# Kernel optimization log

Measured on AMD Instinct MI355X. Metric: run time of the kernel, lower is better.

## Reference

```python
import jax, jax.numpy as jnp
import numpy as np

DIM = 1024
N_HEADS = 16
HEAD_DIM = DIM // N_HEADS
SCALE = HEAD_DIM ** (-0.5)


def setup_inputs() -> dict:
    key = jax.random.key(0)
    ks = jax.random.split(key, 5)
    B, N = 2, 1024
    x = jax.random.normal(ks[0], (B, N, DIM), dtype=jnp.float32)
    # torch nn.Linear convention: weight is (out_features, in_features)
    w_qkvg = jax.random.normal(ks[1], (4 * DIM, DIM), dtype=jnp.float32) * (DIM ** -0.5)
    b_qkvg = jax.random.normal(ks[2], (4 * DIM,), dtype=jnp.float32) * 0.02
    w_proj = jax.random.normal(ks[3], (DIM, DIM), dtype=jnp.float32) * (DIM ** -0.5)
    b_proj = jax.random.normal(ks[4], (DIM,), dtype=jnp.float32) * 0.02
    return {"x": x, "w_qkvg": w_qkvg, "b_qkvg": b_qkvg, "w_proj": w_proj, "b_proj": b_proj}


def reference(x, w_qkvg, b_qkvg, w_proj, b_proj):
    B, N, dim = x.shape
    # fused qkvg projection: (B, N, 4*dim)
    qkvg = x @ w_qkvg.T + b_qkvg
    # (B, N, 4, H, hd) -> (4, B, H, N, hd)
    qkvg = qkvg.reshape(B, N, 4, N_HEADS, HEAD_DIM).transpose(2, 0, 3, 1, 4)
    q = jax.nn.softplus(qkvg[0])          # (B, H, N, hd)
    k = jax.nn.softplus(qkvg[1])          # (B, H, N, hd)
    v = jax.nn.gelu(qkvg[2], approximate=False)  # (B, H, N, hd)
    g = jax.nn.gelu(qkvg[3], approximate=False)  # (B, H, N, hd)
    # kv = k @ v^T over head_dim -> (B, H, N, N)
    kv = jnp.einsum('bhnd,bhmd->bhnm', k, v)
    # z: contract q over tokens with per-token k-sums -> (B, H, hd)
    z = jnp.einsum('bhcn,bhc->bhn', q, k.sum(axis=-1)) * SCALE
    z = 1.0 / (z + dim)
    # out[b,h,d,n] = sum_c q[b,h,c,n] * kv[b,h,c,d] -> (B, H, N, hd)
    out = jnp.einsum('bhcn,bhcd->bhdn', q, kv) * SCALE
    out = (out + v) * z[:, :, None, :]    # broadcast z over token axis
    out = out.reshape(B, N, dim)          # raw reshape, faithful to original
    out = out * g.reshape(B, N, dim)
    out = out @ w_proj.T + b_proj
    return out
```

## Files before the change

### kernel.cpp

```cpp
#include <hip/hip_runtime.h>
#include <hip/hip_bf16.h>
#include <math.h>

typedef float f32x4 __attribute__((ext_vector_type(4)));
typedef __bf16 bf16_t;
typedef bf16_t bf16x8 __attribute__((ext_vector_type(8)));
typedef bf16_t bf16x4 __attribute__((ext_vector_type(4)));

__device__ __forceinline__ void gload_lds16(const bf16_t* g, bf16_t* l) {
    __builtin_amdgcn_global_load_lds(
        (const __attribute__((address_space(1))) unsigned int*)g,
        (__attribute__((address_space(3))) unsigned int*)l, 16, 0, 0);
}

template<int N_IMM>
__device__ __forceinline__ void wait_vmcnt() {
    if constexpr (N_IMM == 0) asm volatile("s_waitcnt vmcnt(0)" ::: "memory");
    else if constexpr (N_IMM == 1) asm volatile("s_waitcnt vmcnt(1)" ::: "memory");
    else if constexpr (N_IMM == 2) asm volatile("s_waitcnt vmcnt(2)" ::: "memory");
    else if constexpr (N_IMM == 3) asm volatile("s_waitcnt vmcnt(3)" ::: "memory");
    else if constexpr (N_IMM == 4) asm volatile("s_waitcnt vmcnt(4)" ::: "memory");
    else static_assert(N_IMM <= 4, "unsupported vmcnt");
}

__global__ __launch_bounds__(256) void cvt3(const float* __restrict__ a, bf16_t* __restrict__ ao, int na4,
                                            const float* __restrict__ b, bf16_t* __restrict__ bo, int nb4,
                                            const float* __restrict__ c, bf16_t* __restrict__ co, int nc4) {
    int q = blockIdx.x * 256 + threadIdx.x;
    const float* src; bf16_t* dst;
    if (q < na4)            { src = a + (size_t)q * 4;              dst = ao + (size_t)q * 4; }
    else if (q < na4 + nb4) { int r = q - na4; src = b + (size_t)r * 4; dst = bo + (size_t)r * 4; }
    else if (q < na4 + nb4 + nc4) { int r = q - na4 - nb4; src = c + (size_t)r * 4; dst = co + (size_t)r * 4; }
    else return;
    float4 v = *reinterpret_cast<const float4*>(src);
    bf16x4 o;
    o[0] = (bf16_t)v.x; o[1] = (bf16_t)v.y; o[2] = (bf16_t)v.z; o[3] = (bf16_t)v.w;
    *reinterpret_cast<bf16x4*>(dst) = o;
}

template<int BM, int BN, int MR, int NR, int EPI>
__global__ __launch_bounds__(256) void gemm_bt(const bf16_t* __restrict__ A,
                                               const bf16_t* __restrict__ B,
                                               const float* __restrict__ bias,
                                               void* __restrict__ Cout,
                                               int M, int N, int K) {
    constexpr int WCOLS = BN / (NR * 16);
    constexpr int WROWS = BM / (MR * 16);
    static_assert(WROWS * WCOLS == 4, "4 waves");
    constexpr int ASEG = BM / 64, BSEG = BN / 64;
    constexpr int LOADS = ASEG + BSEG;
    __shared__ bf16_t As[2][BM * 32];
    __shared__ bf16_t Bs[2][BN * 32];
    const int tid = threadIdx.x;
    const int lane = tid & 63;
    const int w = tid >> 6;
    const int wr = w / WCOLS, wc = w % WCOLS;
    const int NTM = M / BM;
    const int bid = blockIdx.x;
    const int m0 = (bid % NTM) * BM, n0 = (bid / NTM) * BN;
    const int l15 = lane & 15, lg = lane >> 4;
    const int srow = lane >> 2, pos = lane & 3;

    f32x4 acc[MR][NR] = {};
    const int TNUM = K / 32;

    auto stage = [&](int buf, int k0) {
#pragma unroll
        for (int t = 0; t < ASEG; ++t) {
            int s = w + t * 4;
            int row = s * 16 + srow;
            int ch = pos ^ ((row >> 1) & 3);
            gload_lds16(&A[(size_t)(m0 + row) * K + k0 + ch * 8], &As[buf][s * 512]);
        }
#pragma unroll
        for (int t = 0; t < BSEG; ++t) {
            int s = w + t * 4;
            int row = s * 16 + srow;
            int ch = pos ^ ((row >> 1) & 3);
            gload_lds16(&B[(size_t)(n0 + row) * K + k0 + ch * 8], &Bs[buf][s * 512]);
        }
    };

    stage(0, 0);
    int cur = 0;
    for (int t = 0; t < TNUM; ++t) {
        if (t + 1 < TNUM) {
            stage(cur ^ 1, (t + 1) * 32);
            wait_vmcnt<LOADS>();
        } else {
            wait_vmcnt<0>();
        }
        __builtin_amdgcn_s_barrier();
        __builtin_amdgcn_sched_barrier(0);

        const bf16_t* Ac = As[cur];
        const bf16_t* Bc = Bs[cur];
        bf16x8 af[MR], bfr[NR];
#pragma unroll
        for (int i = 0; i < MR; ++i) {
            int ar = wr * MR * 16 + i * 16 + l15;
            af[i] = *(const bf16x8*)(&Ac[ar * 32 + (lg ^ ((ar >> 1) & 3)) * 8]);
        }
#pragma unroll
        for (int j = 0; j < NR; ++j) {
            int br = wc * NR * 16 + j * 16 + l15;
            bfr[j] = *(const bf16x8*)(&Bc[br * 32 + (lg ^ ((br >> 1) & 3)) * 8]);
        }
#pragma unroll
        for (int i = 0; i < MR; ++i)
#pragma unroll
            for (int j = 0; j < NR; ++j)
                acc[i][j] = __builtin_amdgcn_mfma_f32_16x16x32_bf16(af[i], bfr[j], acc[i][j], 0, 0, 0);
        __builtin_amdgcn_sched_barrier(0);
        __builtin_amdgcn_s_barrier();
        cur ^= 1;
    }

#pragma unroll
    for (int i = 0; i < MR; ++i) {
        int gm_base = m0 + wr * MR * 16 + i * 16 + lg * 4;
#pragma unroll
        for (int j = 0; j < NR; ++j) {
            int gn = n0 + wc * NR * 16 + j * 16 + l15;
            float bv = bias[gn];
#pragma unroll
            for (int r = 0; r < 4; ++r) {
                int gm = gm_base + r;
                float v = acc[i][j][r] + bv;
                if (EPI == 0) {
                    float a;
                    if ((gn >> 10) < 2) {
                        a = fmaxf(v, 0.f) + log1pf(expf(-fabsf(v)));
                    } else {
                        a = 0.5f * v * (1.f + erff(v * 0.70710678118654752f));
                    }
                    ((bf16_t*)Cout)[(size_t)gm * N + gn] = (bf16_t)a;
                } else {
                    ((float*)Cout)[(size_t)gm * N + gn] = v;
                }
            }
        }
    }
}

__global__ __launch_bounds__(256) void attn_A(const bf16_t* __restrict__ qkvg,
                                              float* __restrict__ Apart) {
    const int bh = blockIdx.x;
    const int p = blockIdx.y;
    const int b = bh >> 4, h = bh & 15;
    const int tid = threadIdx.x;
    __shared__ float ks[32][64];
    __shared__ float qs[32][64];
    float acc[4][4] = {};
    const int dg = tid >> 4, eg = tid & 15;
    const int stok = tid >> 3, se0 = (tid & 7) * 8;
    const size_t base = ((size_t)b * 1024) * 4096 + (size_t)h * 64;

    for (int t0 = p * 128; t0 < p * 128 + 128; t0 += 32) {
        __syncthreads();
        size_t rowb = base + (size_t)(t0 + stok) * 4096;
        bf16x8 qv8 = *(const bf16x8*)(&qkvg[rowb + se0]);
        bf16x8 kv8 = *(const bf16x8*)(&qkvg[rowb + 1024 + se0]);
#pragma unroll
        for (int jj = 0; jj < 8; ++jj) {
            qs[stok][se0 + jj] = (float)qv8[jj];
            ks[stok][se0 + jj] = (float)kv8[jj];
        }
        __syncthreads();
#pragma unroll 8
        for (int tt = 0; tt < 32; ++tt) {
            f32x4 kv = *(const f32x4*)(&ks[tt][dg * 4]);
            f32x4 qv = *(const f32x4*)(&qs[tt][eg * 4]);
#pragma unroll
            for (int i = 0; i < 4; ++i)
#pragma unroll
                for (int j = 0; j < 4; ++j) acc[i][j] += kv[i] * qv[j];
        }
    }
    float* dst = Apart + ((size_t)p * 32 + bh) * 4096;
#pragma unroll
    for (int i = 0; i < 4; ++i)
#pragma unroll
        for (int j = 0; j < 4; ++j)
            dst[(dg * 4 + i) * 64 + eg * 4 + j] = acc[i][j];
}

__global__ __launch_bounds__(256) void reduce_A_z(const float* __restrict__ Apart,
                                                  float* __restrict__ A,
                                                  float* __restrict__ z) {
    const int bh = blockIdx.x;
    const int tid = threadIdx.x;
    __shared__ float As[4096];
    for (int i0 = tid * 4; i0 < 4096; i0 += 1024) {
        f32x4 s = {};
#pragma unroll
        for (int p = 0; p < 8; ++p) {
            f32x4 v = *(const f32x4*)(&Apart[((size_t)p * 32 + bh) * 4096 + i0]);
            s += v;
        }
        *(f32x4*)(&As[i0]) = s;
        *(f32x4*)(&A[(size_t)bh * 4096 + i0]) = s;
    }
    __syncthreads();
    if (tid < 64) {
        float s = 0.f;
#pragma unroll 8
        for (int d = 0; d < 64; ++d) s += As[d * 64 + tid];
        z[bh * 64 + tid] = 1.0f / (s * 0.125f + 1024.0f);
    }
}

__global__ __launch_bounds__(256) void out_Y(const bf16_t* __restrict__ qkvg,
                                             const float* __restrict__ A,
                                             const float* __restrict__ z,
                                             bf16_t* __restrict__ Y) {
    const int bh = blockIdx.x;
    const int b = bh >> 4, h = bh & 15;
    const int chunk = blockIdx.y;
    const int tid = threadIdx.x;
    __shared__ float As[64][64];
    __shared__ float vs[32][64];
    __shared__ float zs[64];
    for (int i = tid; i < 4096; i += 256) As[i >> 6][i & 63] = A[(size_t)bh * 4096 + i];
    if (tid < 64) zs[tid] = z[bh * 64 + tid];
    const size_t base = ((size_t)b * 1024) * 4096 + (size_t)h * 64;
    const int e = tid & 63, trow = tid >> 6;
    const int stok = tid >> 3, se0 = (tid & 7) * 8;

    for (int t0 = chunk * 64; t0 < chunk * 64 + 64; t0 += 32) {
        __syncthreads();
        bf16x8 vv8 = *(const bf16x8*)(&qkvg[base + (size_t)(t0 + stok) * 4096 + 2048 + se0]);
#pragma unroll
        for (int jj = 0; jj < 8; ++jj) vs[stok][se0 + jj] = (float)vv8[jj];
        __syncthreads();
#pragma unroll
        for (int kk = 0; kk < 8; ++kk) {
            int ml = trow * 8 + kk;
            int m = t0 + ml;
            float s = 0.f;
#pragma unroll 8
            for (int d = 0; d < 64; ++d) s += vs[ml][d] * As[d][e];
            float g = (float)qkvg[base + (size_t)m * 4096 + 3072 + e];
            float o = (s * 0.125f + vs[ml][e]) * zs[e] * g;
            Y[((size_t)b * 1024 + h * 64 + (m >> 4)) * 1024 + ((m & 15) << 6) + e] = (bf16_t)o;
        }
    }
}

extern "C" void kernel_launch(void* const* d_in, const int* in_sizes, int n_in,
                              void* d_out, int out_size, void* d_ws, size_t ws_size,
                              hipStream_t stream) {
    const float* x      = (const float*)d_in[0];
    const float* w_qkvg = (const float*)d_in[1];
    const float* b_qkvg = (const float*)d_in[2];
    const float* w_proj = (const float*)d_in[3];
    const float* b_proj = (const float*)d_in[4];

    char* p = (char*)d_ws;
    bf16_t* xb    = (bf16_t*)p; p += (size_t)2048 * 1024 * 2;
    bf16_t* w1b   = (bf16_t*)p; p += (size_t)4096 * 1024 * 2;
    bf16_t* w2b   = (bf16_t*)p; p += (size_t)1024 * 1024 * 2;
    bf16_t* qkvg  = (bf16_t*)p; p += (size_t)2048 * 4096 * 2;
    float*  Apart = (float*)p;  p += (size_t)8 * 32 * 4096 * 4;
    float*  Afull = (float*)p;  p += (size_t)32 * 4096 * 4;
    float*  zbuf  = (float*)p;  p += (size_t)32 * 64 * 4;
    bf16_t* Ybuf  = (bf16_t*)p; p += (size_t)2048 * 1024 * 2;

    cvt3<<<7168, 256, 0, stream>>>(x, xb, 524288, w_qkvg, w1b, 1048576, w_proj, w2b, 262144);

    gemm_bt<128, 64, 4, 2, 0><<<16 * 64, 256, 0, stream>>>(xb, w1b, b_qkvg, (void*)qkvg, 2048, 4096, 1024);
    attn_A<<<dim3(32, 8), 256, 0, stream>>>(qkvg, Apart);
    reduce_A_z<<<32, 256, 0, stream>>>(Apart, Afull, zbuf);
    out_Y<<<dim3(32, 16), 256, 0, stream>>>(qkvg, Afull, zbuf, Ybuf);
    gemm_bt<64, 64, 2, 2, 1><<<32 * 16, 256, 0, stream>>>(Ybuf, w2b, b_proj, d_out, 2048, 1024, 1024);
}
```

Before: 101.8 us.

## Deepen GEMM pipeline to four LDS stages, swizzle block order, enlarge QKVG tile

The GEMM's double-buffered LDS pipeline becomes a four-buffer ring that prefetches three K-steps ahead. It waits on vmcnt for the oldest stage and drops the trailing barrier per iteration. Block indices are remapped into 8x8 tile groups so neighbouring blocks share A/B rows in L2. The QKVG projection tile grows from 128x64 to 128x128, which raises register and LDS use per block and may lower occupancy.

New measurement: 158.4 us. 55.6% more time.

```diff
diff --git a/kernel.cpp b/kernel.cpp
--- a/kernel.cpp
+++ b/kernel.cpp
@@ -20,7 +20,10 @@
     else if constexpr (N_IMM == 2) asm volatile("s_waitcnt vmcnt(2)" ::: "memory");
     else if constexpr (N_IMM == 3) asm volatile("s_waitcnt vmcnt(3)" ::: "memory");
     else if constexpr (N_IMM == 4) asm volatile("s_waitcnt vmcnt(4)" ::: "memory");
-    else static_assert(N_IMM <= 4, "unsupported vmcnt");
+    else if constexpr (N_IMM == 6) asm volatile("s_waitcnt vmcnt(6)" ::: "memory");
+    else if constexpr (N_IMM == 8) asm volatile("s_waitcnt vmcnt(8)" ::: "memory");
+    else if constexpr (N_IMM == 12) asm volatile("s_waitcnt vmcnt(12)" ::: "memory");
+    else static_assert(N_IMM == 0, "unsupported vmcnt");
 }
 
 __global__ __launch_bounds__(256) void cvt3(const float* __restrict__ a, bf16_t* __restrict__ ao, int na4,
@@ -49,15 +52,21 @@
     static_assert(WROWS * WCOLS == 4, "4 waves");
     constexpr int ASEG = BM / 64, BSEG = BN / 64;
     constexpr int LOADS = ASEG + BSEG;
-    __shared__ bf16_t As[2][BM * 32];
-    __shared__ bf16_t Bs[2][BN * 32];
+    __shared__ bf16_t As[4][BM * 32];
+    __shared__ bf16_t Bs[4][BN * 32];
     const int tid = threadIdx.x;
     const int lane = tid & 63;
     const int w = tid >> 6;
     const int wr = w / WCOLS, wc = w % WCOLS;
+
     const int NTM = M / BM;
-    const int bid = blockIdx.x;
-    const int m0 = (bid % NTM) * BM, n0 = (bid / NTM) * BN;
+    const int c = blockIdx.x & 7;
+    const int pp = blockIdx.x >> 3;
+    const int CHM = NTM >> 3;
+    const int cm = c % CHM, cn = c / CHM;
+    const int mt = cm * 8 + (pp & 7), nt = cn * 8 + (pp >> 3);
+    const int m0 = mt * BM, n0 = nt * BN;
+
     const int l15 = lane & 15, lg = lane >> 4;
     const int srow = lane >> 2, pos = lane & 3;
 
@@ -81,20 +90,18 @@
         }
     };
 
-    stage(0, 0);
-    int cur = 0;
+    stage(0, 0); stage(1, 32); stage(2, 64);
     for (int t = 0; t < TNUM; ++t) {
-        if (t + 1 < TNUM) {
-            stage(cur ^ 1, (t + 1) * 32);
-            wait_vmcnt<LOADS>();
-        } else {
-            wait_vmcnt<0>();
-        }
+        int rem = TNUM - 1 - t;
+        if (rem >= 2)       wait_vmcnt<2 * LOADS>();
+        else if (rem == 1)  wait_vmcnt<LOADS>();
+        else                wait_vmcnt<0>();
         __builtin_amdgcn_s_barrier();
         __builtin_amdgcn_sched_barrier(0);
-
-        const bf16_t* Ac = As[cur];
-        const bf16_t* Bc = Bs[cur];
+        if (t + 3 < TNUM) stage((t + 3) & 3, (t + 3) * 32);
+
+        const bf16_t* Ac = As[t & 3];
+        const bf16_t* Bc = Bs[t & 3];
         bf16x8 af[MR], bfr[NR];
 #pragma unroll
         for (int i = 0; i < MR; ++i) {
@@ -112,8 +119,6 @@
             for (int j = 0; j < NR; ++j)
                 acc[i][j] = __builtin_amdgcn_mfma_f32_16x16x32_bf16(af[i], bfr[j], acc[i][j], 0, 0, 0);
         __builtin_amdgcn_sched_barrier(0);
-        __builtin_amdgcn_s_barrier();
-        cur ^= 1;
     }
 
 #pragma unroll
@@ -268,9 +273,9 @@
 
     cvt3<<<7168, 256, 0, stream>>>(x, xb, 524288, w_qkvg, w1b, 1048576, w_proj, w2b, 262144);
 
-    gemm_bt<128, 64, 4, 2, 0><<<16 * 64, 256, 0, stream>>>(xb, w1b, b_qkvg, (void*)qkvg, 2048, 4096, 1024);
+    gemm_bt<128, 128, 4, 4, 0><<<512, 256, 0, stream>>>(xb, w1b, b_qkvg, (void*)qkvg, 2048, 4096, 1024);
     attn_A<<<dim3(32, 8), 256, 0, stream>>>(qkvg, Apart);
     reduce_A_z<<<32, 256, 0, stream>>>(Apart, Afull, zbuf);
     out_Y<<<dim3(32, 16), 256, 0, stream>>>(qkvg, Afull, zbuf, Ybuf);
-    gemm_bt<64, 64, 2, 2, 1><<<32 * 16, 256, 0, stream>>>(Ybuf, w2b, b_proj, d_out, 2048, 1024, 1024);
-}
+    gemm_bt<64, 64, 2, 2, 1><<<512, 256, 0, stream>>>(Ybuf, w2b, b_proj, d_out, 2048, 1024, 1024);
+}
```

## Replace QKVG GEMM with 512-thread 128x256 tile kernel and XCD-aware block mapping

Applied to the files above, without the earlier changes.

Adds a dedicated gemm8 kernel for the QKVG projection. It uses 8 waves, 128x256 output tiles and a K-step of 64 with an XOR-swizzled LDS layout, so each block reuses its operands across more MFMAs and fewer blocks are launched. Both GEMMs now remap block IDs so that the blocks landing on each of the 8 XCDs cover a contiguous sub-grid of tiles, which is meant to improve L2 locality. The risks are higher register and LDS pressure, which lowers occupancy, and only 256 blocks on the large GEMM, which may leave some CUs underused.

Result: slower. 155.2 us (+52.4%).

```diff
diff --git a/kernel.cpp b/kernel.cpp
--- a/kernel.cpp
+++ b/kernel.cpp
@@ -16,11 +16,10 @@
 template<int N_IMM>
 __device__ __forceinline__ void wait_vmcnt() {
     if constexpr (N_IMM == 0) asm volatile("s_waitcnt vmcnt(0)" ::: "memory");
-    else if constexpr (N_IMM == 1) asm volatile("s_waitcnt vmcnt(1)" ::: "memory");
     else if constexpr (N_IMM == 2) asm volatile("s_waitcnt vmcnt(2)" ::: "memory");
     else if constexpr (N_IMM == 3) asm volatile("s_waitcnt vmcnt(3)" ::: "memory");
     else if constexpr (N_IMM == 4) asm volatile("s_waitcnt vmcnt(4)" ::: "memory");
-    else static_assert(N_IMM <= 4, "unsupported vmcnt");
+    else static_assert(N_IMM == 0, "unsupported vmcnt");
 }
 
 __global__ __launch_bounds__(256) void cvt3(const float* __restrict__ a, bf16_t* __restrict__ ao, int na4,
@@ -38,11 +37,115 @@
     *reinterpret_cast<bf16x4*>(dst) = o;
 }
 
-template<int BM, int BN, int MR, int NR, int EPI>
+__global__ __launch_bounds__(512) void gemm8(const bf16_t* __restrict__ A,
+                                             const bf16_t* __restrict__ B,
+                                             const float* __restrict__ bias,
+                                             bf16_t* __restrict__ Cout,
+                                             int M, int N, int K) {
+    __shared__ bf16_t As[2][128 * 64];
+    __shared__ bf16_t Bs[2][256 * 64];
+    const int tid = threadIdx.x;
+    const int lane = tid & 63;
+    const int w = tid >> 6;
+    const int wr = w >> 2, wc = w & 3;
+
+    const int c = blockIdx.x & 7;
+    const int pp = blockIdx.x >> 3;
+    const int mt = (c & 1) * 8 + (pp & 7);
+    const int nt = (c >> 1) * 4 + (pp >> 3);
+    const int m0 = mt * 128, n0 = nt * 256;
+
+    const int l15 = lane & 15, lg = lane >> 4;
+    const int srow = lane >> 3;
+    const int slot = lane & 7;
+
+    f32x4 acc[4][4] = {};
+    const int TNUM = K / 64;
+
+    auto stage = [&](int buf, int k0) {
+#pragma unroll
+        for (int t = 0; t < 2; ++t) {
+            int s = w + t * 8;
+            int row = s * 8 + srow;
+            int cg = slot ^ (row & 7);
+            gload_lds16(&A[(size_t)(m0 + row) * K + k0 + cg * 8], &As[buf][s * 512]);
+        }
+#pragma unroll
+        for (int t = 0; t < 4; ++t) {
+            int s = w + t * 8;
+            int row = s * 8 + srow;
+            int cg = slot ^ (row & 7);
+            gload_lds16(&B[(size_t)(n0 + row) * K + k0 + cg * 8], &Bs[buf][s * 512]);
+        }
+    };
+
+    stage(0, 0);
+    wait_vmcnt<0>();
+    __builtin_amdgcn_s_barrier();
+    __builtin_amdgcn_sched_barrier(0);
+
+    int cur = 0;
+    for (int t = 0; t < TNUM; ++t) {
+        if (t + 1 < TNUM) stage(cur ^ 1, (t + 1) * 64);
+
+        const bf16_t* Ac = As[cur];
+        const bf16_t* Bc = Bs[cur];
+#pragma unroll
+        for (int kk = 0; kk < 2; ++kk) {
+            bf16x8 af[4], bfr[4];
+#pragma unroll
+            for (int i = 0; i < 4; ++i) {
+                int ar = wr * 64 + i * 16 + l15;
+                int ch = (kk * 4 + lg) ^ (ar & 7);
+                af[i] = *(const bf16x8*)(&Ac[ar * 64 + ch * 8]);
+            }
+#pragma unroll
+            for (int j = 0; j < 4; ++j) {
+                int br = wc * 64 + j * 16 + l15;
+                int ch = (kk * 4 + lg) ^ (br & 7);
+                bfr[j] = *(const bf16x8*)(&Bc[br * 64 + ch * 8]);
+            }
+#pragma unroll
+            for (int i = 0; i < 4; ++i)
+#pragma unroll
+                for (int j = 0; j < 4; ++j)
+                    acc[i][j] = __builtin_amdgcn_mfma_f32_16x16x32_bf16(af[i], bfr[j], acc[i][j], 0, 0, 0);
+        }
+        __builtin_amdgcn_sched_barrier(0);
+        wait_vmcnt<0>();
+        __builtin_amdgcn_s_barrier();
+        __builtin_amdgcn_sched_barrier(0);
+        cur ^= 1;
+    }
+
+#pragma unroll
+    for (int i = 0; i < 4; ++i) {
+        int gm_base = m0 + wr * 64 + i * 16 + lg * 4;
+#pragma unroll
+        for (int j = 0; j < 4; ++j) {
+            int gn = n0 + wc * 64 + j * 16 + l15;
+            float bv = bias[gn];
+#pragma unroll
+            for (int r = 0; r < 4; ++r) {
+                int gm = gm_base + r;
+                float v = acc[i][j][r] + bv;
+                float a;
+                if ((gn >> 10) < 2) {
+                    a = fmaxf(v, 0.f) + log1pf(expf(-fabsf(v)));
+                } else {
+                    a = 0.5f * v * (1.f + erff(v * 0.70710678118654752f));
+                }
+                Cout[(size_t)gm * N + gn] = (bf16_t)a;
+            }
+        }
+    }
+}
+
+template<int BM, int BN, int MR, int NR>
 __global__ __launch_bounds__(256) void gemm_bt(const bf16_t* __restrict__ A,
                                                const bf16_t* __restrict__ B,
                                                const float* __restrict__ bias,
-                                               void* __restrict__ Cout,
+                                               float* __restrict__ Cout,
                                                int M, int N, int K) {
     constexpr int WCOLS = BN / (NR * 16);
     constexpr int WROWS = BM / (MR * 16);
@@ -55,9 +158,16 @@
     const int lane = tid & 63;
     const int w = tid >> 6;
     const int wr = w / WCOLS, wc = w % WCOLS;
-    const int NTM = M / BM;
-    const int bid = blockIdx.x;
-    const int m0 = (bid % NTM) * BM, n0 = (bid / NTM) * BN;
+
+    const int NTM = M / BM, NTN = N / BN;
+    const int CHM = NTM >> 3;
+    const int chunkN = (NTN * CHM) >> 3;
+    const int c = blockIdx.x & 7;
+    const int pp = blockIdx.x >> 3;
+    const int mt = (c % CHM) * 8 + (pp & 7);
+    const int nt = (c / CHM) * chunkN + (pp >> 3);
+    const int m0 = mt * BM, n0 = nt * BN;
+
     const int l15 = lane & 15, lg = lane >> 4;
     const int srow = lane >> 2, pos = lane & 3;
 
@@ -126,18 +236,7 @@
 #pragma unroll
             for (int r = 0; r < 4; ++r) {
                 int gm = gm_base + r;
-                float v = acc[i][j][r] + bv;
-                if (EPI == 0) {
-                    float a;
-                    if ((gn >> 10) < 2) {
-                        a = fmaxf(v, 0.f) + log1pf(expf(-fabsf(v)));
-                    } else {
-                        a = 0.5f * v * (1.f + erff(v * 0.70710678118654752f));
-                    }
-                    ((bf16_t*)Cout)[(size_t)gm * N + gn] = (bf16_t)a;
-                } else {
-                    ((float*)Cout)[(size_t)gm * N + gn] = v;
-                }
+                Cout[(size_t)gm * N + gn] = acc[i][j][r] + bv;
             }
         }
     }
@@ -268,9 +367,9 @@
 
     cvt3<<<7168, 256, 0, stream>>>(x, xb, 524288, w_qkvg, w1b, 1048576, w_proj, w2b, 262144);
 
-    gemm_bt<128, 64, 4, 2, 0><<<16 * 64, 256, 0, stream>>>(xb, w1b, b_qkvg, (void*)qkvg, 2048, 4096, 1024);
+    gemm8<<<256, 512, 0, stream>>>(xb, w1b, b_qkvg, qkvg, 2048, 4096, 1024);
     attn_A<<<dim3(32, 8), 256, 0, stream>>>(qkvg, Apart);
     reduce_A_z<<<32, 256, 0, stream>>>(Apart, Afull, zbuf);
     out_Y<<<dim3(32, 16), 256, 0, stream>>>(qkvg, Afull, zbuf, Ybuf);
-    gemm_bt<64, 64, 2, 2, 1><<<32 * 16, 256, 0, stream>>>(Ybuf, w2b, b_proj, d_out, 2048, 1024, 1024);
-}
+    gemm_bt<64, 64, 2, 2><<<512, 256, 0, stream>>>(Ybuf, w2b, b_proj, (float*)d_out, 2048, 1024, 1024);
+}
```

## Split QKVG GEMM per projection with XCD-aware tile swizzle and specialized epilogues

Applied to the files above, without the earlier changes.

Replaces the single 128x64-tile QKVG GEMM launch with four 64x64-tile launches, one per q/k/v/g slice. Each launch writes into the interleaved output through a new ldc stride and uses a compile-time epilogue (softplus or GELU) in place of a per-element branch. It also remaps block IDs so that each of the 8 blockIdx&7 groups gets a contiguous chunk of M and N tiles, aiming for better L2 locality per XCD. The trade-off is smaller tiles with less operand reuse, plus three extra kernel launches.

After: 131.3 us. 1.29x slower.

```diff
diff --git a/kernel.cpp b/kernel.cpp
--- a/kernel.cpp
+++ b/kernel.cpp
@@ -16,11 +16,10 @@
 template<int N_IMM>
 __device__ __forceinline__ void wait_vmcnt() {
     if constexpr (N_IMM == 0) asm volatile("s_waitcnt vmcnt(0)" ::: "memory");
-    else if constexpr (N_IMM == 1) asm volatile("s_waitcnt vmcnt(1)" ::: "memory");
     else if constexpr (N_IMM == 2) asm volatile("s_waitcnt vmcnt(2)" ::: "memory");
     else if constexpr (N_IMM == 3) asm volatile("s_waitcnt vmcnt(3)" ::: "memory");
     else if constexpr (N_IMM == 4) asm volatile("s_waitcnt vmcnt(4)" ::: "memory");
-    else static_assert(N_IMM <= 4, "unsupported vmcnt");
+    else static_assert(N_IMM == 0, "unsupported vmcnt");
 }
 
 __global__ __launch_bounds__(256) void cvt3(const float* __restrict__ a, bf16_t* __restrict__ ao, int na4,
@@ -43,7 +42,7 @@
                                                const bf16_t* __restrict__ B,
                                                const float* __restrict__ bias,
                                                void* __restrict__ Cout,
-                                               int M, int N, int K) {
+                                               int M, int N, int K, int ldc) {
     constexpr int WCOLS = BN / (NR * 16);
     constexpr int WROWS = BM / (MR * 16);
     static_assert(WROWS * WCOLS == 4, "4 waves");
@@ -55,9 +54,16 @@
     const int lane = tid & 63;
     const int w = tid >> 6;
     const int wr = w / WCOLS, wc = w % WCOLS;
-    const int NTM = M / BM;
-    const int bid = blockIdx.x;
-    const int m0 = (bid % NTM) * BM, n0 = (bid / NTM) * BN;
+
+    const int NTM = M / BM, NTN = N / BN;
+    const int CHM = NTM >> 3;
+    const int chunkN = (NTN * CHM) >> 3;
+    const int c = blockIdx.x & 7;
+    const int pp = blockIdx.x >> 3;
+    const int mt = (c % CHM) * 8 + (pp & 7);
+    const int nt = (c / CHM) * chunkN + (pp >> 3);
+    const int m0 = mt * BM, n0 = nt * BN;
+
     const int l15 = lane & 15, lg = lane >> 4;
     const int srow = lane >> 2, pos = lane & 3;
 
@@ -128,15 +134,13 @@
                 int gm = gm_base + r;
                 float v = acc[i][j][r] + bv;
                 if (EPI == 0) {
-                    float a;
-                    if ((gn >> 10) < 2) {
-                        a = fmaxf(v, 0.f) + log1pf(expf(-fabsf(v)));
-                    } else {
-                        a = 0.5f * v * (1.f + erff(v * 0.70710678118654752f));
-                    }
-                    ((bf16_t*)Cout)[(size_t)gm * N + gn] = (bf16_t)a;
+                    float a = fmaxf(v, 0.f) + log1pf(expf(-fabsf(v)));
+                    ((bf16_t*)Cout)[(size_t)gm * ldc + gn] = (bf16_t)a;
+                } else if (EPI == 1) {
+                    float a = 0.5f * v * (1.f + erff(v * 0.70710678118654752f));
+                    ((bf16_t*)Cout)[(size_t)gm * ldc + gn] = (bf16_t)a;
                 } else {
-                    ((float*)Cout)[(size_t)gm * N + gn] = v;
+                    ((float*)Cout)[(size_t)gm * ldc + gn] = v;
                 }
             }
         }
@@ -268,9 +272,17 @@
 
     cvt3<<<7168, 256, 0, stream>>>(x, xb, 524288, w_qkvg, w1b, 1048576, w_proj, w2b, 262144);
 
-    gemm_bt<128, 64, 4, 2, 0><<<16 * 64, 256, 0, stream>>>(xb, w1b, b_qkvg, (void*)qkvg, 2048, 4096, 1024);
+    gemm_bt<64, 64, 2, 2, 0><<<512, 256, 0, stream>>>(xb, w1b + (size_t)0 * 1024 * 1024,
+        b_qkvg + 0 * 1024, (void*)(qkvg + 0 * 1024), 2048, 1024, 1024, 4096);
+    gemm_bt<64, 64, 2, 2, 0><<<512, 256, 0, stream>>>(xb, w1b + (size_t)1 * 1024 * 1024,
+        b_qkvg + 1 * 1024, (void*)(qkvg + 1 * 1024), 2048, 1024, 1024, 4096);
+    gemm_bt<64, 64, 2, 2, 1><<<512, 256, 0, stream>>>(xb, w1b + (size_t)2 * 1024 * 1024,
+        b_qkvg + 2 * 1024, (void*)(qkvg + 2 * 1024), 2048, 1024, 1024, 4096);
+    gemm_bt<64, 64, 2, 2, 1><<<512, 256, 0, stream>>>(xb, w1b + (size_t)3 * 1024 * 1024,
+        b_qkvg + 3 * 1024, (void*)(qkvg + 3 * 1024), 2048, 1024, 1024, 4096);
+
     attn_A<<<dim3(32, 8), 256, 0, stream>>>(qkvg, Apart);
     reduce_A_z<<<32, 256, 0, stream>>>(Apart, Afull, zbuf);
     out_Y<<<dim3(32, 16), 256, 0, stream>>>(qkvg, Afull, zbuf, Ybuf);
-    gemm_bt<64, 64, 2, 2, 1><<<32 * 16, 256, 0, stream>>>(Ybuf, w2b, b_proj, d_out, 2048, 1024, 1024);
-}
+    gemm_bt<64, 64, 2, 2, 2><<<512, 256, 0, stream>>>(Ybuf, w2b, b_proj, d_out, 2048, 1024, 1024, 1024);
+}
```
